# Kernel optimization log

Measured on AMD Instinct MI355X. Metric: run time of the kernel, lower is better.

The kernel has to match this reference:

```python
import jax, jax.numpy as jnp
import numpy as np

N = 20000      # nodes
E = 80000      # edges (before self loops)
NG = 64        # graphs in batch
EMB = 780      # embedding_size (768 text + 12 time)
NEG_SLOPE = 0.2
BN_EPS = 1e-5


def setup_inputs() -> dict:
    key = jax.random.key(0)
    ks = jax.random.split(key, 20)
    def rn(k, shape, s=0.05):
        return jax.random.normal(k, shape, dtype=jnp.float32) * s
    z = lambda n: jnp.zeros((n,), dtype=jnp.float32)
    o = lambda n: jnp.ones((n,), dtype=jnp.float32)
    x = jax.random.normal(ks[0], (N, 772), dtype=jnp.float32)
    edge_index = jax.random.randint(ks[1], (2, E), 0, N)
    batch = jnp.sort(jax.random.randint(ks[2], (N,), 0, NG))
    return dict(
        x=x, edge_index=edge_index, batch=batch,
        time_W=rn(ks[3], (4, 12)), time_b=z(12),
        lin_W0=rn(ks[4], (EMB, 3 * EMB)), att_src0=rn(ks[5], (3, EMB)), att_dst0=rn(ks[6], (3, EMB)),
        bias0=z(3 * EMB), gamma0=o(3 * EMB), beta0=z(3 * EMB),
        lin_W1=rn(ks[7], (3 * EMB, 3 * EMB)), att_src1=rn(ks[8], (3, EMB)), att_dst1=rn(ks[9], (3, EMB)),
        bias1=z(3 * EMB), gamma1=o(3 * EMB), beta1=z(3 * EMB),
        lin_W2=rn(ks[10], (3 * EMB, EMB)), att_src2=rn(ks[11], (1, EMB)), att_dst2=rn(ks[12], (1, EMB)),
        bias2=z(EMB), gamma2=o(EMB), beta2=z(EMB),
        mlp_W1=rn(ks[13], (EMB, 128)), mlp_b1=z(128),
        mlp_W2=rn(ks[14], (128, 64)), mlp_b2=z(64),
    )


def _gat_layer(h, src, dst, W, a_src, a_dst, b, heads):
    # PyG GATConv (eval mode: dropout off), concat=True, self loops already in src/dst
    C = W.shape[1] // heads
    hp = (h @ W).reshape(N, heads, C)                       # [N,H,C]
    a_s = jnp.sum(hp * a_src[None], axis=-1)                # [N,H]
    a_d = jnp.sum(hp * a_dst[None], axis=-1)                # [N,H]
    e = jax.nn.leaky_relu(a_s[src] + a_d[dst], NEG_SLOPE)   # [E+N,H]
    m = jax.ops.segment_max(e, dst, num_segments=N)         # segment softmax over incoming edges
    m = jnp.where(jnp.isfinite(m), m, 0.0)
    p = jnp.exp(e - m[dst])
    denom = jax.ops.segment_sum(p, dst, num_segments=N)
    alpha = p / (denom[dst] + 1e-16)                        # [E+N,H]
    out = jax.ops.segment_sum(alpha[:, :, None] * hp[src], dst, num_segments=N)  # [N,H,C]
    return out.reshape(N, heads * C) + b


def _bn(h, gamma, beta):
    # BatchNorm in training-mode math (batch statistics, biased variance)
    mu = jnp.mean(h, axis=0)
    var = jnp.mean((h - mu) ** 2, axis=0)
    return (h - mu) * jax.lax.rsqrt(var + BN_EPS) * gamma + beta


def reference(x, edge_index, batch, time_W, time_b,
              lin_W0, att_src0, att_dst0, bias0, gamma0, beta0,
              lin_W1, att_src1, att_dst1, bias1, gamma1, beta1,
              lin_W2, att_src2, att_dst2, bias2, gamma2, beta2,
              mlp_W1, mlp_b1, mlp_W2, mlp_b2):
    te = x[:, 768:772] @ time_W + time_b
    h = jnp.concatenate([jax.lax.stop_gradient(x[:, :768]), te,
                         jax.lax.stop_gradient(x[:, 772:])], axis=-1)  # [N, 780]
    sl = jnp.arange(N)
    src = jnp.concatenate([edge_index[0], sl])   # add self loops
    dst = jnp.concatenate([edge_index[1], sl])
    layers = [
        (lin_W0, att_src0, att_dst0, bias0, gamma0, beta0, 3),
        (lin_W1, att_src1, att_dst1, bias1, gamma1, beta1, 3),
        (lin_W2, att_src2, att_dst2, bias2, gamma2, beta2, 1),
    ]
    for W, a_s, a_d, b, g, bt, heads in layers:
        h = jnp.tanh(_gat_layer(h, src, dst, W, a_s, a_d, b, heads))
        h = _bn(h, g, bt)
    cnt = jax.ops.segment_sum(jnp.ones((N,), dtype=h.dtype), batch, num_segments=NG)
    pooled = jax.ops.segment_sum(h, batch, num_segments=NG) / jnp.maximum(cnt, 1.0)[:, None]
    pooled = jax.nn.relu(pooled)
    out = jnp.tanh(pooled @ mlp_W1 + mlp_b1) @ mlp_W2 + mlp_b2
    return out  # [NG, 64]
```

## Files before the change

### kernel.cpp

```cpp
#include <hip/hip_runtime.h>
#include <math.h>

#define NN   20000
#define EE   80000
#define ELP  100000
#define NGR  64
#define EMB  780
#define W3   2340
#define EMBP 832
#define W3P  2368
#define NZ   (W3+8)

static inline int cdiv_i(long long a, long long b){ return (int)((a + b - 1) / b); }

typedef _Float16 f16;
typedef _Float16 f16x4 __attribute__((ext_vector_type(4)));
typedef _Float16 f16x8 __attribute__((ext_vector_type(8)));
typedef float    f32x4 __attribute__((ext_vector_type(4)));

__device__ __forceinline__ void async_ld16(const f16* g, f16* l){
    __builtin_amdgcn_global_load_lds(
        (const __attribute__((address_space(1))) unsigned int*)g,
        (__attribute__((address_space(3))) unsigned int*)l,
        16, 0, 0);
}

__global__ void k_zero_f32(float* p, int n){
    int i = blockIdx.x*256 + threadIdx.x; if (i < n) p[i] = 0.f;
}
__global__ void k_zero_i32(int* p, int n){
    int i = blockIdx.x*256 + threadIdx.x; if (i < n) p[i] = 0;
}

__global__ void k_transpose(const float* __restrict__ W, f16* __restrict__ Wt,
                            const float* __restrict__ sc, const float* __restrict__ sh,
                            float* __restrict__ dvec, int K, int N, int KP){
    __shared__ float T[32][33];
    __shared__ float D[8][33];
    int n0 = blockIdx.x*32, k0 = blockIdx.y*32;
    int tx = threadIdx.x, ty = threadIdx.y;
    float raw[4];
#pragma unroll
    for (int r = 0; r < 4; r++){
        int k = k0 + ty + r*8;
        float w = 0.f;
        if (k < K && n0 + tx < N) w = W[(size_t)k*N + n0 + tx];
        raw[r] = w;
        T[ty + r*8][tx] = sc ? w * ((k < K) ? sc[k] : 0.f) : w;
    }
    if (sh){
        float p = 0.f;
#pragma unroll
        for (int r = 0; r < 4; r++){
            int k = k0 + ty + r*8;
            if (k < K) p += sh[k] * raw[r];
        }
        D[ty][tx] = p;
    }
    __syncthreads();
#pragma unroll
    for (int r = 0; r < 4; r++){
        int n = n0 + ty + r*8;
        int k = k0 + tx;
        if (n < N && k < KP) Wt[(size_t)n*KP + k] = (f16)T[tx][ty + r*8];
    }
    if (sh && ty == 0 && n0 + tx < N){
        float s = 0.f;
#pragma unroll
        for (int j = 0; j < 8; j++) s += D[j][tx];
        atomicAdd(&dvec[n0 + tx], s);
    }
}

__global__ void k_wvec(const float* __restrict__ W, const float* __restrict__ asrc,
                       const float* __restrict__ adst, const float* __restrict__ sc,
                       f16* __restrict__ Wt, float* __restrict__ dvec,
                       int K, int N, int KP, int H){
    int k = blockIdx.x*4 + (threadIdx.x >> 6);
    int lane = threadIdx.x & 63;
    if (k < K){
        const float* row = W + (size_t)k*N;
        float acc[6];
#pragma unroll
        for (int i = 0; i < 6; i++) acc[i] = 0.f;
        for (int c = lane; c < EMB; c += 64){
            for (int h = 0; h < H; h++){
                float wv = row[h*EMB + c];
                acc[h]     += wv * asrc[h*EMB + c];
                acc[H + h] += wv * adst[h*EMB + c];
            }
        }
        float s = sc ? sc[k] : 1.f;
        for (int i = 0; i < 2*H; i++){
            float v = acc[i];
#pragma unroll
            for (int off = 32; off; off >>= 1) v += __shfl_xor(v, off);
            if (lane == 0) Wt[(size_t)(N + i)*KP + k] = (f16)(v * s);
        }
    }
    if (blockIdx.x == 0){
        int wv = threadIdx.x >> 6;
        for (int i = wv; i < 2*H; i += 4){
            int h = (i < H) ? i : (i - H);
            const float* att = (i < H) ? (asrc + h*EMB) : (adst + h*EMB);
            float s = 0.f;
            for (int c = lane; c < EMB; c += 64) s += dvec[h*EMB + c] * att[c];
#pragma unroll
            for (int off = 32; off; off >>= 1) s += __shfl_xor(s, off);
            if (lane == 0) dvec[N + i] = s;
        }
    }
}

__global__ void k_build_h(const float* __restrict__ x, const float* __restrict__ tW,
                          const float* __restrict__ tb, f16* __restrict__ h){
    int idx = blockIdx.x*256 + threadIdx.x;
    int total = NN*(EMBP/4);
    if (idx >= total) return;
    int n = idx / (EMBP/4);
    int c0 = (idx - n*(EMBP/4))*4;
    const float* xr = x + (size_t)n*772;
    f16x4 o;
#pragma unroll
    for (int j = 0; j < 4; j++){
        int c = c0 + j; float v;
        if (c < 768) v = xr[c];
        else if (c < EMB){
            int t = c - 768;
            v = tb[t] + xr[768]*tW[t] + xr[769]*tW[12+t] + xr[770]*tW[24+t] + xr[771]*tW[36+t];
        } else v = 0.f;
        o[j] = (f16)v;
    }
    *(f16x4*)(h + (size_t)n*EMBP + c0) = o;
}

__global__ void k_deg(const int* __restrict__ ei, int* __restrict__ deg){
    int k = blockIdx.x*256 + threadIdx.x; if (k >= ELP) return;
    int d = (k < EE) ? ei[EE + k] : (k - EE);
    atomicAdd(&deg[d], 1);
}

__global__ __launch_bounds__(1024) void k_scan(int* __restrict__ deg, int* __restrict__ rp){
    __shared__ int part[1024];
    int tid = threadIdx.x;
    int i0 = tid*20;
    int n = (i0 < NN) ? min(20, NN - i0) : 0;
    int s = 0;
    for (int k = 0; k < n; k++) s += deg[i0+k];
    part[tid] = s; __syncthreads();
    for (int off = 1; off < 1024; off <<= 1){
        int t = (tid >= off) ? part[tid-off] : 0;
        __syncthreads();
        part[tid] += t;
        __syncthreads();
    }
    int run = part[tid] - s;
    for (int k = 0; k < n; k++){
        int d = deg[i0+k];
        rp[i0+k] = run;
        deg[i0+k] = run;
        run += d;
    }
    if (tid == 1023) rp[NN] = part[1023];
}

__global__ void k_fill(const int* __restrict__ ei, int* __restrict__ cursor, int* __restrict__ csrc){
    int k = blockIdx.x*256 + threadIdx.x; if (k >= ELP) return;
    int s, d;
    if (k < EE){ s = ei[k]; d = ei[EE + k]; } else { s = k - EE; d = s; }
    int pos = atomicAdd(&cursor[d], 1);
    csrc[pos] = s;
}

__global__ void k_grp(const int* __restrict__ batch, int* __restrict__ grp){
    int g = blockIdx.x*256 + threadIdx.x; if (g > NGR) return;
    int lo = 0, hi = NN;
    while (lo < hi){ int mid = (lo+hi)>>1; if (batch[mid] < g) lo = mid+1; else hi = mid; }
    grp[g] = lo;
}

__global__ __launch_bounds__(512, 2) void k_gemm8(const f16* __restrict__ A,
                                                  const f16* __restrict__ Bt,
                                                  const float* __restrict__ dvec,
                                                  f16* __restrict__ C,
                                                  float* __restrict__ a_sd,
                                                  int M, int N, int NB, int H,
                                                  int KP, int SN, int Mtiles, int NT){
    __shared__ f16 sA[65536];
    f16* sB = sA + 32768;

    int nwg = Mtiles*NT;
    int bid = blockIdx.x;
    int q = nwg >> 3, r = nwg & 7, xcd = bid & 7, lin = bid >> 3;
    int wg = (xcd < r ? xcd*(q+1) : r*(q+1) + (xcd - r)*q) + lin;
    int mt = wg / NT, nt = wg - mt*NT;
    int m0 = mt*256, n0 = nt*256;

    int tid = threadIdx.x;
    int w = tid >> 6, lane = tid & 63;
    int lm = lane & 15, lq = lane >> 4;
    int wm = w >> 2, wn = w & 3;

    int rstage0 = w*32 + (lane >> 2);
    int rstage1 = rstage0 + 16;
    int kqs = ((lane & 3) ^ ((lane >> 3) & 3)) * 8;
    const f16* gA0 = A  + (size_t)min(m0 + rstage0, M-1)*KP + kqs;
    const f16* gA1 = A  + (size_t)min(m0 + rstage1, M-1)*KP + kqs;
    const f16* gB0 = Bt + (size_t)min(n0 + rstage0, NB-1)*KP + kqs;
    const f16* gB1 = Bt + (size_t)min(n0 + rstage1, NB-1)*KP + kqs;
    int so0 = w*1024, so1 = w*1024 + 512;

    int swz  = (lq ^ ((lm >> 1) & 3)) * 8;
    int aoff = (wm*128 + lm)*32 + swz;
    int boff = (wn*64  + lm)*32 + swz;

    f32x4 acc[8][4];
#pragma unroll
    for (int i = 0; i < 8; i++)
#pragma unroll
        for (int j = 0; j < 4; j++) acc[i][j] = (f32x4)0.f;

    int KT = KP >> 6;

    async_ld16(gA0,      &sA[so0]);         async_ld16(gA1,      &sA[so1]);
    async_ld16(gB0,      &sB[so0]);         async_ld16(gB1,      &sB[so1]);
    async_ld16(gA0 + 32, &sA[8192+so0]);    async_ld16(gA1 + 32, &sA[8192+so1]);
    async_ld16(gB0 + 32, &sB[8192+so0]);    async_ld16(gB1 + 32, &sB[8192+so1]);
    async_ld16(gA0 + 64, &sA[16384+so0]);   async_ld16(gA1 + 64, &sA[16384+so1]);
    async_ld16(gB0 + 64, &sB[16384+so0]);   async_ld16(gB1 + 64, &sB[16384+so1]);
    asm volatile("s_waitcnt vmcnt(4)" ::: "memory");
    __builtin_amdgcn_s_barrier();

    for (int t = 0; t < KT; t++){
        int buf  = (t & 1) << 14;
        int nbuf = buf ^ 16384;
        bool s1 = (t+1 < KT), s2 = (t+2 < KT);
        int ko1 = (t+1)*64, ko2 = (t+2)*64;
        f16x8 aF[4], bF[4];

#pragma unroll
        for (int i = 0; i < 4; i++) aF[i] = *(const f16x8*)&sA[buf + aoff + i*512];
#pragma unroll
        for (int i = 0; i < 4; i++) bF[i] = *(const f16x8*)&sB[buf + boff + i*512];
        if (s1){ async_ld16(gA0+ko1+32, &sA[nbuf+8192+so0]); async_ld16(gA1+ko1+32, &sA[nbuf+8192+so1]); }
        __builtin_amdgcn_s_setprio(1);
#pragma unroll
        for (int i = 0; i < 4; i++)
#pragma unroll
            for (int j = 0; j < 4; j++)
                acc[i][j] = __builtin_amdgcn_mfma_f32_16x16x32_f16(aF[i], bF[j], acc[i][j], 0, 0, 0);
        __builtin_amdgcn_s_setprio(0);
        __builtin_amdgcn_s_barrier();

#pragma unroll
        for (int i = 0; i < 4; i++) aF[i] = *(const f16x8*)&sA[buf + aoff + 2048 + i*512];
        if (s1){ async_ld16(gB0+ko1+32, &sB[nbuf+8192+so0]); async_ld16(gB1+ko1+32, &sB[nbuf+8192+so1]); }
        __builtin_amdgcn_s_setprio(1);
#pragma unroll
        for (int i = 0; i < 4; i++)
#pragma unroll
            for (int j = 0; j < 4; j++)
                acc[4+i][j] = __builtin_amdgcn_mfma_f32_16x16x32_f16(aF[i], bF[j], acc[4+i][j], 0, 0, 0);
        __builtin_amdgcn_s_setprio(0);
        __builtin_amdgcn_s_barrier();

#pragma unroll
        for (int i = 0; i < 4; i++) aF[i] = *(const f16x8*)&sA[buf + 8192 + aoff + i*512];
#pragma unroll
        for (int i = 0; i < 4; i++) bF[i] = *(const f16x8*)&sB[buf + 8192 + boff + i*512];
        if (s2){ async_ld16(gA0+ko2, &sA[buf+so0]); async_ld16(gA1+ko2, &sA[buf+so1]); }
        __builtin_amdgcn_s_setprio(1);
#pragma unroll
        for (int i = 0; i < 4; i++)
#pragma unroll
            for (int j = 0; j < 4; j++)
                acc[i][j] = __builtin_amdgcn_mfma_f32_16x16x32_f16(aF[i], bF[j], acc[i][j], 0, 0, 0);
        __builtin_amdgcn_s_setprio(0);
        __builtin_amdgcn_s_barrier();

#pragma unroll
        for (int i = 0; i < 4; i++) aF[i] = *(const f16x8*)&sA[buf + 8192 + aoff + 2048 + i*512];
        if (s2){ async_ld16(gB0+ko2, &sB[buf+so0]); async_ld16(gB1+ko2, &sB[buf+so1]); }
        __builtin_amdgcn_s_setprio(1);
#pragma unroll
        for (int i = 0; i < 4; i++)
#pragma unroll
            for (int j = 0; j < 4; j++)
                acc[4+i][j] = __builtin_amdgcn_mfma_f32_16x16x32_f16(aF[i], bF[j], acc[4+i][j], 0, 0, 0);
        __builtin_amdgcn_s_setprio(0);
        if (s2) asm volatile("s_waitcnt vmcnt(4)" ::: "memory");
        else    asm volatile("s_waitcnt vmcnt(0)" ::: "memory");
        __builtin_amdgcn_s_barrier();
    }

#pragma unroll
    for (int mi = 0; mi < 8; mi++){
#pragma unroll
        for (int ni = 0; ni < 4; ni++){
            int col = n0 + wn*64 + ni*16 + lm;
            if (col >= N && col < NB){
                int jc = col - N;
                int idx = (jc < H) ? jc : (3 + jc - H);
                float dv = dvec[col];
                int rbase = m0 + wm*128 + mi*16 + lq*4;
#pragma unroll
                for (int rr = 0; rr < 4; rr++){
                    int row = rbase + rr;
                    if (row < M) a_sd[(size_t)row*6 + idx] = acc[mi][ni][rr] + dv;
                }
            }
        }
    }

    float dv4[4];
#pragma unroll
    for (int ni = 0; ni < 4; ni++){
        int gcol = n0 + wn*64 + ni*16 + lm;
        dv4[ni] = (gcol < N) ? dvec[gcol] : 0.f;
    }
    int ncols = min(256, N - n0);
#pragma unroll
    for (int hh = 0; hh < 2; hh++){
        __builtin_amdgcn_s_barrier();
        if (wm == hh){
#pragma unroll
            for (int mi = 0; mi < 8; mi++){
#pragma unroll
                for (int ni = 0; ni < 4; ni++){
                    int colL = wn*64 + ni*16 + lm;
#pragma unroll
                    for (int rr = 0; rr < 4; rr++){
                        int rowL = mi*16 + lq*4 + rr;
                        sA[rowL*264 + colL] = (f16)(acc[mi][ni][rr] + dv4[ni]);
                    }
                }
            }
        }
        __builtin_amdgcn_s_barrier();
#pragma unroll
        for (int it = 0; it < 8; it++){
            int ch = tid + it*512;
            int rowL = ch >> 5, cc = (ch & 31)*8;
            int grow = m0 + hh*128 + rowL;
            if (grow < M && cc < ncols){
                if (cc + 8 <= ncols){
                    f16x8 v = *(f16x8*)&sA[rowL*264 + cc];
                    *(f16x8*)(C + (size_t)grow*SN + n0 + cc) = v;
                } else {
                    for (int jj = cc; jj < ncols; jj++)
                        C[(size_t)grow*SN + n0 + jj] = sA[rowL*264 + jj];
                }
            }
        }
    }
}

template<int H>
__global__ __launch_bounds__(256) void k_agg2(const f16* __restrict__ hp, const int* __restrict__ rp,
                                              const int* __restrict__ csrc, const float* __restrict__ a_sd,
                                              const float* __restrict__ bias,
                                              f16* __restrict__ y, int SP, int W){
    int n = blockIdx.x, tid = threadIdx.x, lane = tid & 63;
    int beg = rp[n], deg = rp[n+1] - beg;

    float adv[H];
#pragma unroll
    for (int h = 0; h < H; h++) adv[h] = a_sd[(size_t)n*6 + 3 + h];

    float mx[H];
#pragma unroll
    for (int h = 0; h < H; h++) mx[h] = -1e30f;
    for (int base = 0; base < deg; base += 64){
        int e = base + lane;
        if (e < deg){
            int s = csrc[beg + e];
#pragma unroll
            for (int h = 0; h < H; h++){
                float t = a_sd[(size_t)s*6 + h] + adv[h];
                t = t > 0.f ? t : 0.2f*t;
                mx[h] = fmaxf(mx[h], t);
            }
        }
    }
#pragma unroll
    for (int off = 32; off; off >>= 1)
#pragma unroll
        for (int h = 0; h < H; h++) mx[h] = fmaxf(mx[h], __shfl_xor(mx[h], off));

    float dn[H];
#pragma unroll
    for (int h = 0; h < H; h++) dn[h] = 0.f;
    for (int base = 0; base < deg; base += 64){
        int e = base + lane;
        if (e < deg){
            int s = csrc[beg + e];
#pragma unroll
            for (int h = 0; h < H; h++){
                float t = a_sd[(size_t)s*6 + h] + adv[h];
                t = t > 0.f ? t : 0.2f*t;
                dn[h] += expf(t - mx[h]);
            }
        }
    }
#pragma unroll
    for (int off = 32; off; off >>= 1)
#pragma unroll
        for (int h = 0; h < H; h++) dn[h] += __shfl_xor(dn[h], off);
    float inv[H];
#pragma unroll
    for (int h = 0; h < H; h++) inv[h] = 1.f / (dn[h] + 1e-16f);

    float acc[2][8];
#pragma unroll
    for (int g = 0; g < 2; g++)
#pragma unroll
        for (int j = 0; j < 8; j++) acc[g][j] = 0.f;
    int  cg[2];  cg[0] = tid*8; cg[1] = 2048 + tid*8;
    bool act[2]; act[0] = cg[0] < W; act[1] = cg[1] < W;
    int hlo[2], hhi[2], nsp[2];
#pragma unroll
    for (int g = 0; g < 2; g++){
        int c = cg[g];
        int hl = min(c / EMB, H-1);
        int hh = min((c+7) / EMB, H-1);
        hlo[g] = hl; hhi[g] = hh;
        nsp[g] = (hh > hl) ? (EMB*(hl+1) - c) : 8;
    }

    for (int base = 0; base < deg; base += 64){
        int cnt = min(64, deg - base);
        int sl = 0; float al[H];
        {
            int e = base + lane;
            if (e < deg){
                sl = csrc[beg + e];
#pragma unroll
                for (int h = 0; h < H; h++){
                    float t = a_sd[(size_t)sl*6 + h] + adv[h];
                    t = t > 0.f ? t : 0.2f*t;
                    al[h] = expf(t - mx[h]) * inv[h];
                }
            } else {
#pragma unroll
                for (int h = 0; h < H; h++) al[h] = 0.f;
            }
        }
#pragma unroll 4
        for (int e = 0; e < cnt; e++){
            int s = __shfl(sl, e);
            float a0 = __shfl(al[0], e);
            float a1 = (H==3) ? __shfl(al[1], e) : a0;
            float a2 = (H==3) ? __shfl(al[2], e) : a0;
            const f16* row = hp + (size_t)s*SP;
#pragma unroll
            for (int g = 0; g < 2; g++){
                if (act[g]){
                    f16x8 v = *(const f16x8*)(row + cg[g]);
                    float lo = (hlo[g]==0) ? a0 : (hlo[g]==1 ? a1 : a2);
                    float hi = (hhi[g]==0) ? a0 : (hhi[g]==1 ? a1 : a2);
#pragma unroll
                    for (int j = 0; j < 8; j++){
                        float alj = (j < nsp[g]) ? lo : hi;
                        acc[g][j] += alj * (float)v[j];
                    }
                }
            }
        }
    }

#pragma unroll
    for (int g = 0; g < 2; g++){
        int c = cg[g];
        if (c < SP){
            f16x8 o;
#pragma unroll
            for (int j = 0; j < 8; j++){
                float vv = (c + j < W) ? tanhf(acc[g][j] + bias[c+j]) : 0.f;
                o[j] = (f16)vv;
            }
            *(f16x8*)(y + (size_t)n*SP + c) = o;
        }
    }
}

__global__ void k_bnstat(const f16* __restrict__ y, float* __restrict__ ps,
                         float* __restrict__ pq, int W, int SP){
    int c0 = (blockIdx.x*256 + threadIdx.x)*4;
    if (c0 >= W) return;
    int slice = blockIdx.y;
    int r0 = (int)(((long long)NN*slice)/128);
    int r1 = (int)(((long long)NN*(slice+1))/128);
    float s[4] = {0,0,0,0}, q[4] = {0,0,0,0};
    for (int r = r0; r < r1; r++){
        f16x4 u = *(const f16x4*)(y + (size_t)r*SP + c0);
#pragma unroll
        for (int j = 0; j < 4; j++){ float v = (float)u[j]; s[j] += v; q[j] += v*v; }
    }
#pragma unroll
    for (int j = 0; j < 4; j++){
        ps[(size_t)slice*W3 + c0+j] = s[j];
        pq[(size_t)slice*W3 + c0+j] = q[j];
    }
}

__global__ void k_bnfin(const float* __restrict__ ps, const float* __restrict__ pq,
                        const float* __restrict__ gamma, const float* __restrict__ beta,
                        float* __restrict__ sc, float* __restrict__ sh,
                        float* __restrict__ dvec, int W, int zn){
    int c = blockIdx.x*256 + threadIdx.x;
    if (c < W){
        float m = 0.f, q = 0.f;
        for (int s = 0; s < 128; s++){ m += ps[(size_t)s*W3 + c]; q += pq[(size_t)s*W3 + c]; }
        m *= (1.f/NN);
        float v = q * (1.f/NN) - m*m;
        float is = 1.f / sqrtf(v + 1e-5f);
        float g = gamma[c];
        sc[c] = is * g;
        sh[c] = beta[c] - m * is * g;
    }
    if (c < zn) dvec[c] = 0.f;
}

__global__ void k_pool(const f16* __restrict__ h, const int* __restrict__ grp,
                       float* __restrict__ pooled){
    int g = blockIdx.x;
    int c = threadIdx.x*4;
    if (c >= EMB) return;
    int r0 = grp[g], r1 = grp[g+1];
    float s0=0.f, s1=0.f, s2=0.f, s3=0.f;
    for (int r = r0; r < r1; r++){
        f16x4 u = *(const f16x4*)(h + (size_t)r*EMBP + c);
        s0 += (float)u[0]; s1 += (float)u[1]; s2 += (float)u[2]; s3 += (float)u[3];
    }
    pooled[g*EMB + c] = s0; pooled[g*EMB + c+1] = s1;
    pooled[g*EMB + c+2] = s2; pooled[g*EMB + c+3] = s3;
}

__global__ __launch_bounds__(256) void k_mlp(const float* __restrict__ pooled, const int* __restrict__ grp,
                                             const float* __restrict__ sc, const float* __restrict__ sh,
                                             const float* __restrict__ W1, const float* __restrict__ b1,
                                             const float* __restrict__ W2, const float* __restrict__ b2,
                                             float* __restrict__ out){
    __shared__ float p[EMB];
    __shared__ float hid[128];
    int g = blockIdx.x, tid = threadIdx.x;
    int cnt = grp[g+1] - grp[g];
    float ic = 1.f / fmaxf((float)cnt, 1.f);
    for (int c = tid; c < EMB; c += 256){
        float v = pooled[g*EMB + c] * ic * sc[c] + sh[c];
        p[c] = v > 0.f ? v : 0.f;
    }
    __syncthreads();
    if (tid < 128){
        float s = b1[tid];
        for (int k = 0; k < EMB; k++) s += p[k] * W1[k*128 + tid];
        hid[tid] = tanhf(s);
    }
    __syncthreads();
    if (tid < 64){
        float s = b2[tid];
        for (int k = 0; k < 128; k++) s += hid[k] * W2[k*64 + tid];
        out[g*64 + tid] = s;
    }
}

extern "C" void kernel_launch(void* const* d_in, const int* in_sizes, int n_in,
                              void* d_out, int out_size, void* d_ws, size_t ws_size,
                              hipStream_t stream) {
    (void)in_sizes; (void)n_in; (void)out_size;
    const float* x    = (const float*)d_in[0];
    const int*   ei   = (const int*)  d_in[1];
    const int*   batch= (const int*)  d_in[2];
    const float* tW   = (const float*)d_in[3];
    const float* tb   = (const float*)d_in[4];
    const float* W0   = (const float*)d_in[5];
    const float* as0  = (const float*)d_in[6];
    const float* ad0  = (const float*)d_in[7];
    const float* b0   = (const float*)d_in[8];
    const float* g0   = (const float*)d_in[9];
    const float* be0  = (const float*)d_in[10];
    const float* W1   = (const float*)d_in[11];
    const float* as1  = (const float*)d_in[12];
    const float* ad1  = (const float*)d_in[13];
    const float* b1   = (const float*)d_in[14];
    const float* g1   = (const float*)d_in[15];
    const float* be1  = (const float*)d_in[16];
    const float* W2   = (const float*)d_in[17];
    const float* as2  = (const float*)d_in[18];
    const float* ad2  = (const float*)d_in[19];
    const float* b2   = (const float*)d_in[20];
    const float* g2   = (const float*)d_in[21];
    const float* be2  = (const float*)d_in[22];
    const float* mW1  = (const float*)d_in[23];
    const float* mb1  = (const float*)d_in[24];
    const float* mW2  = (const float*)d_in[25];
    const float* mb2  = (const float*)d_in[26];
    float* outp = (float*)d_out;

    size_t off = 0;
    auto carve = [&](size_t bytes) -> void* {
        void* p = (char*)d_ws + off;
        off = (off + bytes + 255) & ~(size_t)255;
        return p;
    };
    f16* big1 = (f16*)carve((size_t)NN*W3P*2);
    f16* big2 = (f16*)carve((size_t)NN*W3P*2);
    f16* Wt   = (f16*)carve((size_t)NZ*W3P*2);
    float* a_sd  = (float*)carve((size_t)NN*6*4);
    float* psum  = (float*)carve((size_t)128*W3*4);
    float* psq   = (float*)carve((size_t)128*W3*4);
    float* sc    = (float*)carve((size_t)W3*4);
    float* sh    = (float*)carve((size_t)W3*4);
    float* dvec  = (float*)carve((size_t)NZ*4);
    float* pooled= (float*)carve((size_t)NGR*EMB*4);
    int*   grp   = (int*)carve((size_t)(NGR+1)*4);
    int*   deg   = (int*)carve((size_t)NN*4);
    int*   rp    = (int*)carve((size_t)(NN+1)*4);
    int*   csrc  = (int*)carve((size_t)ELP*4);

    if (ws_size < off) return;

    k_zero_i32<<<cdiv_i(NN,256),256,0,stream>>>(deg, NN);
    k_deg<<<cdiv_i(ELP,256),256,0,stream>>>(ei, deg);
    k_scan<<<1,1024,0,stream>>>(deg, rp);
    k_fill<<<cdiv_i(ELP,256),256,0,stream>>>(ei, deg, csrc);
    k_grp<<<1,256,0,stream>>>(batch, grp);

    k_build_h<<<cdiv_i((long long)NN*(EMBP/4),256),256,0,stream>>>(x, tW, tb, big1);
    k_zero_f32<<<cdiv_i(NZ,256),256,0,stream>>>(dvec, NZ);

    struct Layer { const float* W; const float* as; const float* ad; const float* b;
                   const float* g; const float* be; int H; int K; int KP; };
    Layer layers[3] = {
        {W0, as0, ad0, b0, g0, be0, 3, EMB, EMBP},
        {W1, as1, ad1, b1, g1, be1, 3, W3,  W3P },
        {W2, as2, ad2, b2, g2, be2, 1, W3,  W3P },
    };

    for (int L = 0; L < 3; L++){
        Layer& ly = layers[L];
        int Wout  = ly.H * EMB;
        int NB    = Wout + 2*ly.H;
        int SPout = (Wout == W3) ? W3P : EMBP;
        const float* scale = (L == 0) ? nullptr : sc;
        const float* shift = (L == 0) ? nullptr : sh;

        dim3 tg(cdiv_i(Wout,32), cdiv_i(ly.KP,32));
        k_transpose<<<tg, dim3(32,8), 0, stream>>>(ly.W, Wt, scale, shift, dvec, ly.K, Wout, ly.KP);
        k_wvec<<<cdiv_i(ly.K,4),256,0,stream>>>(ly.W, ly.as, ly.ad, scale, Wt, dvec, ly.K, Wout, ly.KP, ly.H);

        int Mtiles = cdiv_i(NN,256), NT = cdiv_i(NB,256);
        k_gemm8<<<Mtiles*NT, 512, 0, stream>>>(big1, Wt, dvec, big2, a_sd,
                                               NN, Wout, NB, ly.H, ly.KP, SPout, Mtiles, NT);

        if (ly.H == 3)
            k_agg2<3><<<NN,256,0,stream>>>(big2, rp, csrc, a_sd, ly.b, big1, SPout, Wout);
        else
            k_agg2<1><<<NN,256,0,stream>>>(big2, rp, csrc, a_sd, ly.b, big1, SPout, Wout);

        dim3 gs(cdiv_i(Wout/4,256), 128);
        k_bnstat<<<gs,256,0,stream>>>(big1, psum, psq, Wout, SPout);
        int zn = (L < 2) ? NZ : 0;
        k_bnfin<<<cdiv_i(Wout,256),256,0,stream>>>(psum, psq, ly.g, ly.be, sc, sh, dvec, Wout, zn);
    }

    k_pool<<<NGR,256,0,stream>>>(big1, grp, pooled);
    k_mlp<<<NGR,256,0,stream>>>(pooled, grp, sc, sh, mW1, mb1, mW2, mb2, outp);
}
```

Measured before the change: 1.502 ms.

## Shrink GEMM tile to 128x256 with triple-buffered K=32 pipeline

Replaces the 256x256 GEMM tile, which used a 64-deep K step and double buffering in 128KB LDS, with a 128x256 tile using 32-deep K steps and a three-stage LDS ring of about 72KB. The launch bound rises to 4 waves-per-SIMD occupancy and the epilogue writes the whole tile through LDS in one pass. This doubles the workgroup count and aims for better occupancy and load balance, at the cost of less operand reuse per tile and a barrier after every small K step.

```diff
diff --git a/kernel.cpp b/kernel.cpp
--- a/kernel.cpp
+++ b/kernel.cpp
@@ -179,70 +179,72 @@
     grp[g] = lo;
 }
 
-__global__ __launch_bounds__(512, 2) void k_gemm8(const f16* __restrict__ A,
+__global__ __launch_bounds__(512, 4) void k_gemmT(const f16* __restrict__ A,
                                                   const f16* __restrict__ Bt,
                                                   const float* __restrict__ dvec,
                                                   f16* __restrict__ C,
                                                   float* __restrict__ a_sd,
                                                   int M, int N, int NB, int H,
                                                   int KP, int SN, int Mtiles, int NT){
-    __shared__ f16 sA[65536];
-    f16* sB = sA + 32768;
+    __shared__ f16 smem[36864];
+    f16* sB = smem + 12288;
 
     int nwg = Mtiles*NT;
     int bid = blockIdx.x;
     int q = nwg >> 3, r = nwg & 7, xcd = bid & 7, lin = bid >> 3;
     int wg = (xcd < r ? xcd*(q+1) : r*(q+1) + (xcd - r)*q) + lin;
     int mt = wg / NT, nt = wg - mt*NT;
-    int m0 = mt*256, n0 = nt*256;
+    int m0 = mt*128, n0 = nt*256;
 
     int tid = threadIdx.x;
     int w = tid >> 6, lane = tid & 63;
     int lm = lane & 15, lq = lane >> 4;
     int wm = w >> 2, wn = w & 3;
 
-    int rstage0 = w*32 + (lane >> 2);
-    int rstage1 = rstage0 + 16;
     int kqs = ((lane & 3) ^ ((lane >> 3) & 3)) * 8;
-    const f16* gA0 = A  + (size_t)min(m0 + rstage0, M-1)*KP + kqs;
-    const f16* gA1 = A  + (size_t)min(m0 + rstage1, M-1)*KP + kqs;
-    const f16* gB0 = Bt + (size_t)min(n0 + rstage0, NB-1)*KP + kqs;
-    const f16* gB1 = Bt + (size_t)min(n0 + rstage1, NB-1)*KP + kqs;
-    int so0 = w*1024, so1 = w*1024 + 512;
+    const f16* gA0 = A  + (size_t)min(m0 + w*16 + (lane >> 2), M-1)*KP + kqs;
+    const f16* gB0 = Bt + (size_t)min(n0 + w*32 + (lane >> 2), NB-1)*KP + kqs;
+    const f16* gB1 = Bt + (size_t)min(n0 + w*32 + 16 + (lane >> 2), NB-1)*KP + kqs;
+    int sa0 = w*512;
+    int sb0 = w*1024, sb1 = w*1024 + 512;
 
     int swz  = (lq ^ ((lm >> 1) & 3)) * 8;
-    int aoff = (wm*128 + lm)*32 + swz;
-    int boff = (wn*64  + lm)*32 + swz;
-
-    f32x4 acc[8][4];
-#pragma unroll
-    for (int i = 0; i < 8; i++)
+    int aoff = (wm*64 + lm)*32 + swz;
+    int boff = (wn*64 + lm)*32 + swz;
+
+    f32x4 acc[4][4];
+#pragma unroll
+    for (int i = 0; i < 4; i++)
 #pragma unroll
         for (int j = 0; j < 4; j++) acc[i][j] = (f32x4)0.f;
 
-    int KT = KP >> 6;
-
-    async_ld16(gA0,      &sA[so0]);         async_ld16(gA1,      &sA[so1]);
-    async_ld16(gB0,      &sB[so0]);         async_ld16(gB1,      &sB[so1]);
-    async_ld16(gA0 + 32, &sA[8192+so0]);    async_ld16(gA1 + 32, &sA[8192+so1]);
-    async_ld16(gB0 + 32, &sB[8192+so0]);    async_ld16(gB1 + 32, &sB[8192+so1]);
-    async_ld16(gA0 + 64, &sA[16384+so0]);   async_ld16(gA1 + 64, &sA[16384+so1]);
-    async_ld16(gB0 + 64, &sB[16384+so0]);   async_ld16(gB1 + 64, &sB[16384+so1]);
-    asm volatile("s_waitcnt vmcnt(4)" ::: "memory");
+    int KT = KP >> 5;
+
+    async_ld16(gA0,      &smem[sa0]);
+    async_ld16(gB0,      &sB[sb0]);
+    async_ld16(gB1,      &sB[sb1]);
+    async_ld16(gA0 + 32, &smem[4096 + sa0]);
+    async_ld16(gB0 + 32, &sB[8192 + sb0]);
+    async_ld16(gB1 + 32, &sB[8192 + sb1]);
+    asm volatile("s_waitcnt vmcnt(3)" ::: "memory");
     __builtin_amdgcn_s_barrier();
 
+    int cur = 0, nx2 = 2;
     for (int t = 0; t < KT; t++){
-        int buf  = (t & 1) << 14;
-        int nbuf = buf ^ 16384;
-        bool s1 = (t+1 < KT), s2 = (t+2 < KT);
-        int ko1 = (t+1)*64, ko2 = (t+2)*64;
+        int ac = cur*4096, bc = cur*8192;
         f16x8 aF[4], bF[4];
-
-#pragma unroll
-        for (int i = 0; i < 4; i++) aF[i] = *(const f16x8*)&sA[buf + aoff + i*512];
-#pragma unroll
-        for (int i = 0; i < 4; i++) bF[i] = *(const f16x8*)&sB[buf + boff + i*512];
-        if (s1){ async_ld16(gA0+ko1+32, &sA[nbuf+8192+so0]); async_ld16(gA1+ko1+32, &sA[nbuf+8192+so1]); }
+#pragma unroll
+        for (int i = 0; i < 4; i++) aF[i] = *(const f16x8*)&smem[ac + aoff + i*512];
+#pragma unroll
+        for (int i = 0; i < 4; i++) bF[i] = *(const f16x8*)&sB[bc + boff + i*512];
+        bool s2 = (t+2 < KT);
+        if (s2){
+            int ko2 = (t+2)*32;
+            int a2 = nx2*4096, b2 = nx2*8192;
+            async_ld16(gA0 + ko2, &smem[a2 + sa0]);
+            async_ld16(gB0 + ko2, &sB[b2 + sb0]);
+            async_ld16(gB1 + ko2, &sB[b2 + sb1]);
+        }
         __builtin_amdgcn_s_setprio(1);
 #pragma unroll
         for (int i = 0; i < 4; i++)
@@ -250,51 +252,15 @@
             for (int j = 0; j < 4; j++)
                 acc[i][j] = __builtin_amdgcn_mfma_f32_16x16x32_f16(aF[i], bF[j], acc[i][j], 0, 0, 0);
         __builtin_amdgcn_s_setprio(0);
-        __builtin_amdgcn_s_barrier();
-
-#pragma unroll
-        for (int i = 0; i < 4; i++) aF[i] = *(const f16x8*)&sA[buf + aoff + 2048 + i*512];
-        if (s1){ async_ld16(gB0+ko1+32, &sB[nbuf+8192+so0]); async_ld16(gB1+ko1+32, &sB[nbuf+8192+so1]); }
-        __builtin_amdgcn_s_setprio(1);
-#pragma unroll
-        for (int i = 0; i < 4; i++)
-#pragma unroll
-            for (int j = 0; j < 4; j++)
-                acc[4+i][j] = __builtin_amdgcn_mfma_f32_16x16x32_f16(aF[i], bF[j], acc[4+i][j], 0, 0, 0);
-        __builtin_amdgcn_s_setprio(0);
-        __builtin_amdgcn_s_barrier();
-
-#pragma unroll
-        for (int i = 0; i < 4; i++) aF[i] = *(const f16x8*)&sA[buf + 8192 + aoff + i*512];
-#pragma unroll
-        for (int i = 0; i < 4; i++) bF[i] = *(const f16x8*)&sB[buf + 8192 + boff + i*512];
-        if (s2){ async_ld16(gA0+ko2, &sA[buf+so0]); async_ld16(gA1+ko2, &sA[buf+so1]); }
-        __builtin_amdgcn_s_setprio(1);
-#pragma unroll
-        for (int i = 0; i < 4; i++)
-#pragma unroll
-            for (int j = 0; j < 4; j++)
-                acc[i][j] = __builtin_amdgcn_mfma_f32_16x16x32_f16(aF[i], bF[j], acc[i][j], 0, 0, 0);
-        __builtin_amdgcn_s_setprio(0);
-        __builtin_amdgcn_s_barrier();
-
-#pragma unroll
-        for (int i = 0; i < 4; i++) aF[i] = *(const f16x8*)&sA[buf + 8192 + aoff + 2048 + i*512];
-        if (s2){ async_ld16(gB0+ko2, &sB[buf+so0]); async_ld16(gB1+ko2, &sB[buf+so1]); }
-        __builtin_amdgcn_s_setprio(1);
-#pragma unroll
-        for (int i = 0; i < 4; i++)
-#pragma unroll
-            for (int j = 0; j < 4; j++)
-                acc[4+i][j] = __builtin_amdgcn_mfma_f32_16x16x32_f16(aF[i], bF[j], acc[4+i][j], 0, 0, 0);
-        __builtin_amdgcn_s_setprio(0);
-        if (s2) asm volatile("s_waitcnt vmcnt(4)" ::: "memory");
+        if (s2) asm volatile("s_waitcnt vmcnt(3)" ::: "memory");
         else    asm volatile("s_waitcnt vmcnt(0)" ::: "memory");
         __builtin_amdgcn_s_barrier();
-    }
-
-#pragma unroll
-    for (int mi = 0; mi < 8; mi++){
+        cur = (cur == 2) ? 0 : cur + 1;
+        nx2 = (nx2 == 2) ? 0 : nx2 + 1;
+    }
+
+#pragma unroll
+    for (int mi = 0; mi < 4; mi++){
 #pragma unroll
         for (int ni = 0; ni < 4; ni++){
             int col = n0 + wn*64 + ni*16 + lm;
@@ -302,7 +268,7 @@
                 int jc = col - N;
                 int idx = (jc < H) ? jc : (3 + jc - H);
                 float dv = dvec[col];
-                int rbase = m0 + wm*128 + mi*16 + lq*4;
+                int rbase = m0 + wm*64 + mi*16 + lq*4;
 #pragma unroll
                 for (int rr = 0; rr < 4; rr++){
                     int row = rbase + rr;
@@ -320,36 +286,31 @@
     }
     int ncols = min(256, N - n0);
 #pragma unroll
-    for (int hh = 0; hh < 2; hh++){
-        __builtin_amdgcn_s_barrier();
-        if (wm == hh){
-#pragma unroll
-            for (int mi = 0; mi < 8; mi++){
-#pragma unroll
-                for (int ni = 0; ni < 4; ni++){
-                    int colL = wn*64 + ni*16 + lm;
-#pragma unroll
-                    for (int rr = 0; rr < 4; rr++){
-                        int rowL = mi*16 + lq*4 + rr;
-                        sA[rowL*264 + colL] = (f16)(acc[mi][ni][rr] + dv4[ni]);
-                    }
-                }
-            }
-        }
-        __builtin_amdgcn_s_barrier();
-#pragma unroll
-        for (int it = 0; it < 8; it++){
-            int ch = tid + it*512;
-            int rowL = ch >> 5, cc = (ch & 31)*8;
-            int grow = m0 + hh*128 + rowL;
-            if (grow < M && cc < ncols){
-                if (cc + 8 <= ncols){
-                    f16x8 v = *(f16x8*)&sA[rowL*264 + cc];
-                    *(f16x8*)(C + (size_t)grow*SN + n0 + cc) = v;
-                } else {
-                    for (int jj = cc; jj < ncols; jj++)
-                        C[(size_t)grow*SN + n0 + jj] = sA[rowL*264 + jj];
-                }
+    for (int mi = 0; mi < 4; mi++){
+#pragma unroll
+        for (int ni = 0; ni < 4; ni++){
+            int colL = wn*64 + ni*16 + lm;
+#pragma unroll
+            for (int rr = 0; rr < 4; rr++){
+                int rowL = wm*64 + mi*16 + lq*4 + rr;
+                smem[rowL*264 + colL] = (f16)(acc[mi][ni][rr] + dv4[ni]);
+            }
+        }
+    }
+    asm volatile("s_waitcnt lgkmcnt(0)" ::: "memory");
+    __builtin_amdgcn_s_barrier();
+#pragma unroll
+    for (int it = 0; it < 8; it++){
+        int ch = tid + it*512;
+        int rowL = ch >> 5, cc = (ch & 31)*8;
+        int grow = m0 + rowL;
+        if (grow < M && cc < ncols){
+            if (cc + 8 <= ncols){
+                f16x8 v = *(f16x8*)&smem[rowL*264 + cc];
+                *(f16x8*)(C + (size_t)grow*SN + n0 + cc) = v;
+            } else {
+                for (int jj = cc; jj < ncols; jj++)
+                    C[(size_t)grow*SN + n0 + jj] = smem[rowL*264 + jj];
             }
         }
     }
@@ -649,8 +610,8 @@
         k_transpose<<<tg, dim3(32,8), 0, stream>>>(ly.W, Wt, scale, shift, dvec, ly.K, Wout, ly.KP);
         k_wvec<<<cdiv_i(ly.K,4),256,0,stream>>>(ly.W, ly.as, ly.ad, scale, Wt, dvec, ly.K, Wout, ly.KP, ly.H);
 
-        int Mtiles = cdiv_i(NN,256), NT = cdiv_i(NB,256);
-        k_gemm8<<<Mtiles*NT, 512, 0, stream>>>(big1, Wt, dvec, big2, a_sd,
+        int Mtiles = cdiv_i(NN,128), NT = cdiv_i(NB,256);
+        k_gemmT<<<Mtiles*NT, 512, 0, stream>>>(big1, Wt, dvec, big2, a_sd,
                                                NN, Wout, NB, ly.H, ly.KP, SPout, Mtiles, NT);
 
         if (ly.H == 3)
```

Result: faster. 1.427 ms (-5.0%).
